# Performance work log

Hardware: AMD Instinct MI355X
Metric: run time of the kernel (lower is better)

Reference implementation:

```python
import jax, jax.numpy as jnp
import numpy as np

KS = 3
PAD = 1
STRIDE = 1


def conv2d(x, w, b, stride, pad):
    out = jax.lax.conv_general_dilated(
        x, w, (stride, stride), [(pad, pad), (pad, pad)],
        dimension_numbers=("NCHW", "OIHW", "NCHW"))
    if b is not None:
        out = out + b[None, :, None, None]
    return out


def setup_inputs() -> dict:
    key = jax.random.key(0)
    k = jax.random.split(key, 5)
    b, c, h, w = 4, 64, 128, 128
    return {
        "x0": jax.random.normal(k[0], (b, c, h, w), jnp.float32),
        "x1": jax.random.normal(k[1], (b, c, h, w), jnp.float32),
        "p_w": jax.random.normal(k[2], (2 * KS * KS, c, 3, 3), jnp.float32) * 0.01,
        "p_b": jax.random.normal(k[3], (2 * KS * KS,), jnp.float32) * 0.1,
        "conv_w": jax.random.normal(k[4], (64, c, KS, KS), jnp.float32) * 0.05,
    }


def _deform_forward(x0, x1, p_w, p_b, conv_w):
    ks, N = KS, KS * KS
    offset = conv2d(x1, p_w, p_b, STRIDE, 1)           # (b, 2N, h, w)
    b, _, h, w = offset.shape
    c = x0.shape[1]
    xp = jnp.pad(x0, ((0, 0), (0, 0), (PAD, PAD), (PAD, PAD)))
    Hp, Wp = xp.shape[2], xp.shape[3]

    # kernel-relative offsets p_n and base grid p_0 (1-indexed, as in torch code)
    r = jnp.arange(-(ks - 1) // 2, (ks - 1) // 2 + 1)
    pnx, pny = jnp.meshgrid(r, r, indexing="ij")
    p_n = jnp.concatenate([pnx.ravel(), pny.ravel()]).astype(offset.dtype).reshape(1, 2 * N, 1, 1)
    ax = jnp.arange(1, h * STRIDE + 1, STRIDE)
    ay = jnp.arange(1, w * STRIDE + 1, STRIDE)
    p0x, p0y = jnp.meshgrid(ax, ay, indexing="ij")    # (h, w)
    p_0 = jnp.concatenate([jnp.broadcast_to(p0x, (1, N, h, w)),
                           jnp.broadcast_to(p0y, (1, N, h, w))], 1).astype(offset.dtype)

    p = (p_0 + p_n + offset).transpose(0, 2, 3, 1)     # (b, h, w, 2N)
    q_lt = jnp.floor(jax.lax.stop_gradient(p))
    q_rb = q_lt + 1.0
    qltx = jnp.clip(q_lt[..., :N], 0, Hp - 1).astype(jnp.int32)
    qlty = jnp.clip(q_lt[..., N:], 0, Wp - 1).astype(jnp.int32)
    qrbx = jnp.clip(q_rb[..., :N], 0, Hp - 1).astype(jnp.int32)
    qrby = jnp.clip(q_rb[..., N:], 0, Wp - 1).astype(jnp.int32)
    px = jnp.clip(p[..., :N], 0, Hp - 1)
    py = jnp.clip(p[..., N:], 0, Wp - 1)

    fx_lt = qltx.astype(px.dtype); fy_lt = qlty.astype(px.dtype)
    fx_rb = qrbx.astype(px.dtype); fy_rb = qrby.astype(px.dtype)
    g_lt = (1 + (fx_lt - px)) * (1 + (fy_lt - py))
    g_rb = (1 - (fx_rb - px)) * (1 - (fy_rb - py))
    g_lb = (1 + (fx_lt - px)) * (1 - (fy_rb - py))
    g_rt = (1 - (fx_rb - px)) * (1 + (fy_lt - py))

    x_flat = xp.reshape(b, c, Hp * Wp)

    def gather(qx, qy):
        idx = qx * Wp + qy                              # (b, h, w, N)
        return jax.vmap(lambda xb, ib: xb[:, ib])(x_flat, idx)  # (b, c, h, w, N)

    x_lt = gather(qltx, qlty)
    x_rb = gather(qrbx, qrby)
    x_lb = gather(qltx, qrby)
    x_rt = gather(qrbx, qlty)

    x_off = (g_lt[:, None] * x_lt + g_rb[:, None] * x_rb +
             g_lb[:, None] * x_lb + g_rt[:, None] * x_rt)  # (b, c, h, w, N)

    # (b,c,h,w,ki,kj) -> (b,c,h*ks,w*ks)
    x_off = x_off.reshape(b, c, h, w, ks, ks).transpose(0, 1, 2, 4, 3, 5).reshape(b, c, h * ks, w * ks)
    return conv2d(x_off, conv_w, None, ks, 0)


def reference(x0, x1, p_w, p_b, conv_w):
    return _deform_forward(x0, x1, p_w, p_b, conv_w)
```

## Files before the change

### kernel.cpp

```cpp
#include <hip/hip_runtime.h>

#define BATCH 4
#define CH    64
#define HH    128
#define WW    128
#define HW    (HH*WW)
#define HP    130
#define NOFF  18
#define OC    64

typedef _Float16 half8 __attribute__((ext_vector_type(8)));
typedef _Float16 half2t __attribute__((ext_vector_type(2)));
typedef float f32x4 __attribute__((ext_vector_type(4)));

#define WF_OFF  0
#define PF_OFF  73728
#define X0T_OFF 110592
#define X1T_OFF 8763392
#define REC_OFF 17416192

__global__ __launch_bounds__(256) void prep_all(
    const float* __restrict__ x0, const float* __restrict__ x1,
    const float* __restrict__ cw, const float* __restrict__ pw,
    _Float16* __restrict__ x0t, _Float16* __restrict__ x1t,
    _Float16* __restrict__ wf, _Float16* __restrict__ pf) {
  int blk = blockIdx.x, tid = threadIdx.x;
  if (blk < 2048) {
    __shared__ float tile[64 * 66];
    int jh = blk & 1, i = (blk >> 1) & 127, b = (blk >> 8) & 3, which = blk >> 10;
    const float* src = which ? x1 : x0;
    _Float16* dst = which ? x1t : x0t;
#pragma unroll
    for (int it = 0; it < 4; it++) {
      int idx = it * 256 + tid;
      int c = idx >> 4, j4 = (idx & 15) << 2;
      float4 v = *(const float4*)(src + (size_t)(b * CH + c) * HW + i * WW + jh * 64 + j4);
      *(float4*)&tile[c * 66 + j4] = v;
    }
    __syncthreads();
    int jl = tid >> 2, cq = (tid & 3) << 4;
    _Float16* dp = dst + ((size_t)(b * HP + i + 1) * HP + (jh * 64 + jl + 1)) * CH + cq;
#pragma unroll
    for (int h = 0; h < 2; h++) {
      half8 v;
#pragma unroll
      for (int cc = 0; cc < 8; cc++) v[cc] = (_Float16)tile[(cq + h * 8 + cc) * 66 + jl];
      *(half8*)(dp + h * 8) = v;
    }
    if (tid < 8) {
      int jo = jh ? (HP - 1) : 0;
      _Float16* zp = dst + ((size_t)(b * HP + i + 1) * HP + jo) * CH + tid * 8;
      int4 z = {0, 0, 0, 0};
      *(int4*)zp = z;
    }
  } else if (blk < 2064) {
    int z = blk - 2048;
    int which = z >> 3, b = (z >> 1) & 3, top = z & 1;
    _Float16* dst = (which ? x1t : x0t) + ((size_t)(b * HP + top * (HP - 1)) * HP) * CH;
    int4 zz = {0, 0, 0, 0};
    for (int e = tid; e < 1040; e += 256) *(int4*)((char*)dst + e * 16) = zz;
  } else {
    int gid = (blk - 2064) * 256 + tid;
    if (gid < 36864) {
      int j = gid & 7, lane = (gid >> 3) & 63, mt = (gid >> 9) & 3, s = gid >> 11;
      int oc = mt * 16 + (lane & 15);
      int t = s * 32 + (lane >> 4) * 8 + j;
      int k = t >> 6, c = t & 63;
      wf[gid] = (_Float16)cw[(oc * CH + c) * 9 + k];
    } else {
      int g = gid - 36864;
      int j = g & 7, lane = (g >> 3) & 63, mt = (g >> 9) & 1, s = g >> 10;
      int o = mt * 16 + (lane & 15);
      int t = s * 32 + (lane >> 4) * 8 + j;
      int k = t >> 6, c = t & 63;
      pf[g] = (o < NOFF) ? (_Float16)pw[(o * CH + c) * 9 + k] : (_Float16)0.f;
    }
  }
}

__global__ __launch_bounds__(256, 4) void offset_recs(
    const _Float16* __restrict__ x1t, const _Float16* __restrict__ pf,
    const float* __restrict__ pb, int4* __restrict__ recs) {
  __shared__ _Float16 x1s[3 * 66 * 72];
  __shared__ float offs_lds[64 * 20];
  int blk = blockIdx.x;
  int jh2 = blk & 1, i = (blk >> 1) & 127, b = blk >> 8;
  int j0 = jh2 * 64;
  int tid = threadIdx.x, lane = tid & 63, nt = tid >> 6;
  const _Float16* x1b = x1t + (size_t)b * HP * HP * CH;

#pragma unroll
  for (int it = 0; it < 7; it++) {
    int tau = it * 256 + tid;
    if (tau < 1584) {
      int ki = tau / 528, r2 = tau - ki * 528;
      int col = r2 >> 3, cg = r2 & 7;
      half8 v = *(const half8*)(x1b + ((size_t)(i + ki) * HP + (j0 + col)) * CH + cg * 8);
      *(half8*)&x1s[(ki * 66 + col) * 72 + cg * 8] = v;
    }
  }
  __syncthreads();

  int p = lane & 15, q = lane >> 4;
  const half8* pfv = (const half8*)pf;
  f32x4 acc0 = {0.f, 0.f, 0.f, 0.f}, acc1 = {0.f, 0.f, 0.f, 0.f};
#pragma unroll 3
  for (int s = 0; s < 18; s++) {
    int u = 4 * s + q, k = u >> 3, c0 = (u & 7) << 3;
    int ki = (k * 86) >> 8, kj = k - ki * 3;
    half8 bfrag = *(const half8*)&x1s[(ki * 66 + nt * 16 + p + kj) * 72 + c0];
    acc0 = __builtin_amdgcn_mfma_f32_16x16x32_f16(pfv[(s * 2 + 0) * 64 + lane], bfrag, acc0, 0, 0, 0);
    acc1 = __builtin_amdgcn_mfma_f32_16x16x32_f16(pfv[(s * 2 + 1) * 64 + lane], bfrag, acc1, 0, 0, 0);
  }
  int col = lane & 15, quad = lane >> 4;
  int px = nt * 16 + col;
#pragma unroll
  for (int r = 0; r < 4; r++) {
    int o = quad * 4 + r;
    offs_lds[px * 20 + o] = acc0[r] + pb[o];
    int o2 = 16 + o;
    if (o2 < NOFF) offs_lds[px * 20 + o2] = acc1[r] + pb[o2];
  }
  __syncthreads();

  int px2 = tid >> 2, kg = tid & 3;
  int jj = j0 + px2;
#pragma unroll
  for (int t = 0; t < 3; t++) {
    int k = kg + t * 4;
    if (k <= 8) {
      float ox = offs_lds[px2 * 20 + k], oy = offs_lds[px2 * 20 + k + 9];
      int ki = (k * 86) >> 8, kj = k - ki * 3;
      float pxr = (float)(i + ki) + ox;
      float pyr = (float)(jj + kj) + oy;
      float fx = floorf(pxr), fy = floorf(pyr);
      float qltx = fminf(fmaxf(fx, 0.f), 129.f);
      float qlty = fminf(fmaxf(fy, 0.f), 129.f);
      float qrbx = fminf(fmaxf(fx + 1.f, 0.f), 129.f);
      float qrby = fminf(fmaxf(fy + 1.f, 0.f), 129.f);
      float pxc = fminf(fmaxf(pxr, 0.f), 129.f);
      float pyc = fminf(fmaxf(pyr, 0.f), 129.f);
      float glt = (1.f + qltx - pxc) * (1.f + qlty - pyc);
      float grb = (1.f - qrbx + pxc) * (1.f - qrby + pyc);
      float glb = (1.f + qltx - pxc) * (1.f - qrby + pyc);
      float grt = (1.f - qrbx + pxc) * (1.f + qlty - pyc);
      int4 rec;
      rec.x = (int)qltx | ((int)qlty << 16);
      rec.y = (int)qrbx | ((int)qrby << 16);
      half2t gA = {(_Float16)glt, (_Float16)grb};
      half2t gB = {(_Float16)glb, (_Float16)grt};
      rec.z = __builtin_bit_cast(int, gA);
      rec.w = __builtin_bit_cast(int, gB);
      recs[(size_t)((b * HH + i) * WW + jj) * 9 + k] = rec;
    }
  }
}

__global__ __launch_bounds__(256, 4) void deform_fused(
    const _Float16* __restrict__ x0t, const int4* __restrict__ recs,
    const _Float16* __restrict__ wf, float* __restrict__ out) {
  __shared__ __align__(16) _Float16 btile[2 * 18 * 64 * 8];

  int xcd = blockIdx.x & 7, local = blockIdx.x >> 3;
  int strip = xcd * 256 + local;
  int jq2 = strip & 3, i = (strip >> 2) & 127, b = strip >> 9;
  int j0 = jq2 * 32;
  int tid = threadIdx.x;
  const _Float16* x0b = x0t + (size_t)b * HP * HP * CH;

  {
    int cg = tid & 7, px = tid >> 3;
    int c0 = cg * 8;
    int nt = px >> 4, pxl = px & 15, kgq = cg & 3, sh = cg >> 2;
    const int4* recp = recs + (size_t)((b * HH + i) * WW + (j0 + px)) * 9;
    _Float16* wslot = &btile[(((nt * 18) * 4 + kgq) * 16 + pxl) * 8];
#pragma unroll
    for (int k = 0; k < 9; k++) {
      int4 rec = recp[k];
      int ltx = rec.x & 0xffff, lty = (int)((unsigned)rec.x >> 16);
      int rbx = rec.y & 0xffff, rby = (int)((unsigned)rec.y >> 16);
      const _Float16* rowl = x0b + (size_t)ltx * (HP * CH) + c0;
      const _Float16* rowr = x0b + (size_t)rbx * (HP * CH) + c0;
      half8 vlt = *(const half8*)(rowl + lty * CH);
      half8 vlb = *(const half8*)(rowl + rby * CH);
      half8 vrb = *(const half8*)(rowr + rby * CH);
      half8 vrt = *(const half8*)(rowr + lty * CH);
      half2t gA = __builtin_bit_cast(half2t, rec.z);
      half2t gB = __builtin_bit_cast(half2t, rec.w);
      half8 f = vlt * gA.x + vrb * gA.y + vlb * gB.x + vrt * gB.y;
      int s = k * 2 + sh;
      *(half8*)(wslot + s * 512) = f;
    }
  }
  __syncthreads();

  {
    int lane = tid & 63, w = tid >> 6;
    int nt = w & 1, mt0 = (w >> 1) * 2;
    f32x4 acc0 = {0.f, 0.f, 0.f, 0.f}, acc1 = {0.f, 0.f, 0.f, 0.f};
    const half8* wfv = (const half8*)wf;
    const half8* bt = (const half8*)&btile[nt * (18 * 512)];
#pragma unroll 6
    for (int s = 0; s < 18; s++) {
      half8 bfrag = bt[s * 64 + lane];
      acc0 = __builtin_amdgcn_mfma_f32_16x16x32_f16(wfv[(s * 4 + mt0) * 64 + lane], bfrag, acc0, 0, 0, 0);
      acc1 = __builtin_amdgcn_mfma_f32_16x16x32_f16(wfv[(s * 4 + mt0 + 1) * 64 + lane], bfrag, acc1, 0, 0, 0);
    }
    int col = lane & 15, quad = lane >> 4;
    int jo = j0 + nt * 16 + col;
#pragma unroll
    for (int r = 0; r < 4; r++) {
      int oc0 = mt0 * 16 + quad * 4 + r;
      int oc1 = (mt0 + 1) * 16 + quad * 4 + r;
      out[((b * OC + oc0) * HH + i) * WW + jo] = acc0[r];
      out[((b * OC + oc1) * HH + i) * WW + jo] = acc1[r];
    }
  }
}

extern "C" void kernel_launch(void* const* d_in, const int* in_sizes, int n_in,
                              void* d_out, int out_size, void* d_ws, size_t ws_size,
                              hipStream_t stream) {
  const float* x0 = (const float*)d_in[0];
  const float* x1 = (const float*)d_in[1];
  const float* pw = (const float*)d_in[2];
  const float* pb = (const float*)d_in[3];
  const float* cw = (const float*)d_in[4];
  float* out = (float*)d_out;

  _Float16* wfrag  = (_Float16*)((char*)d_ws + WF_OFF);
  _Float16* pwfrag = (_Float16*)((char*)d_ws + PF_OFF);
  _Float16* x0t    = (_Float16*)((char*)d_ws + X0T_OFF);
  _Float16* x1t    = (_Float16*)((char*)d_ws + X1T_OFF);
  int4*     recs   = (int4*)((char*)d_ws + REC_OFF);

  prep_all<<<dim3(2280), dim3(256), 0, stream>>>(x0, x1, cw, pw, x0t, x1t, wfrag, pwfrag);
  offset_recs<<<dim3(1024), dim3(256), 0, stream>>>(x1t, pwfrag, pb, recs);
  deform_fused<<<dim3(2048), dim3(256), 0, stream>>>(x0t, recs, wfrag, out);
}
```

Measured before the change: 120.9 us.

## Fuse offset convolution and bilinear record computation into deform kernel

Merges the offset-conv/record kernel into the deform kernel. Each block first computes the 18 offset channels for its 32-pixel strip with MFMA, reading x1 fragments straight from global memory instead of staging them in LDS. It then computes the bilinear indices and weights in registers before gathering. This removes one kernel launch and the write and read-back of the int4 records. The costs are redundant per-thread bilinear math (each of the 8 channel-group threads recomputes it), uncached global reads of x1 for the conv, and more work per block.

```diff
diff --git a/kernel.cpp b/kernel.cpp
--- a/kernel.cpp
+++ b/kernel.cpp
@@ -10,14 +10,12 @@
 #define OC    64
 
 typedef _Float16 half8 __attribute__((ext_vector_type(8)));
-typedef _Float16 half2t __attribute__((ext_vector_type(2)));
 typedef float f32x4 __attribute__((ext_vector_type(4)));
 
 #define WF_OFF  0
 #define PF_OFF  73728
 #define X0T_OFF 110592
 #define X1T_OFF 8763392
-#define REC_OFF 17416192
 
 __global__ __launch_bounds__(256) void prep_all(
     const float* __restrict__ x0, const float* __restrict__ x1,
@@ -78,61 +76,58 @@
   }
 }
 
-__global__ __launch_bounds__(256, 4) void offset_recs(
-    const _Float16* __restrict__ x1t, const _Float16* __restrict__ pf,
-    const float* __restrict__ pb, int4* __restrict__ recs) {
-  __shared__ _Float16 x1s[3 * 66 * 72];
-  __shared__ float offs_lds[64 * 20];
-  int blk = blockIdx.x;
-  int jh2 = blk & 1, i = (blk >> 1) & 127, b = blk >> 8;
-  int j0 = jh2 * 64;
-  int tid = threadIdx.x, lane = tid & 63, nt = tid >> 6;
+__global__ __launch_bounds__(256, 4) void deform_all(
+    const _Float16* __restrict__ x0t, const _Float16* __restrict__ x1t,
+    const _Float16* __restrict__ pf, const float* __restrict__ pb,
+    const _Float16* __restrict__ wf, float* __restrict__ out) {
+  __shared__ __align__(16) _Float16 btile[2 * 18 * 64 * 8];
+  __shared__ float offs[32 * 20];
+
+  int xcd = blockIdx.x & 7, local = blockIdx.x >> 3;
+  int strip = xcd * 256 + local;
+  int jq2 = strip & 3, i = (strip >> 2) & 127, b = strip >> 9;
+  int j0 = jq2 * 32;
+  int tid = threadIdx.x;
+  const _Float16* x0b = x0t + (size_t)b * HP * HP * CH;
   const _Float16* x1b = x1t + (size_t)b * HP * HP * CH;
 
+  {
+    int lane = tid & 63, w = tid >> 6;
+    int nt = w & 1, mt = w >> 1;
+    int p = lane & 15, q = lane >> 4;
+    int j = j0 + nt * 16 + p;
+    const half8* pfv = (const half8*)pf;
+    f32x4 acc = {0.f, 0.f, 0.f, 0.f};
+#pragma unroll 3
+    for (int s = 0; s < 18; s++) {
+      int u = 4 * s + q, k = u >> 3, c0 = (u & 7) << 3;
+      int ki = (k * 86) >> 8, kj = k - ki * 3;
+      half8 bfrag = *(const half8*)(x1b + ((size_t)(i + ki) * HP + (j + kj)) * CH + c0);
+      acc = __builtin_amdgcn_mfma_f32_16x16x32_f16(pfv[(s * 2 + mt) * 64 + lane], bfrag, acc, 0, 0, 0);
+    }
+    int col = lane & 15, quad = lane >> 4;
+    int px = nt * 16 + col;
 #pragma unroll
-  for (int it = 0; it < 7; it++) {
-    int tau = it * 256 + tid;
-    if (tau < 1584) {
-      int ki = tau / 528, r2 = tau - ki * 528;
-      int col = r2 >> 3, cg = r2 & 7;
-      half8 v = *(const half8*)(x1b + ((size_t)(i + ki) * HP + (j0 + col)) * CH + cg * 8);
-      *(half8*)&x1s[(ki * 66 + col) * 72 + cg * 8] = v;
+    for (int r = 0; r < 4; r++) {
+      int o = mt * 16 + quad * 4 + r;
+      if (o < NOFF) offs[px * 20 + o] = acc[r] + pb[o];
     }
   }
   __syncthreads();
 
-  int p = lane & 15, q = lane >> 4;
-  const half8* pfv = (const half8*)pf;
-  f32x4 acc0 = {0.f, 0.f, 0.f, 0.f}, acc1 = {0.f, 0.f, 0.f, 0.f};
-#pragma unroll 3
-  for (int s = 0; s < 18; s++) {
-    int u = 4 * s + q, k = u >> 3, c0 = (u & 7) << 3;
-    int ki = (k * 86) >> 8, kj = k - ki * 3;
-    half8 bfrag = *(const half8*)&x1s[(ki * 66 + nt * 16 + p + kj) * 72 + c0];
-    acc0 = __builtin_amdgcn_mfma_f32_16x16x32_f16(pfv[(s * 2 + 0) * 64 + lane], bfrag, acc0, 0, 0, 0);
-    acc1 = __builtin_amdgcn_mfma_f32_16x16x32_f16(pfv[(s * 2 + 1) * 64 + lane], bfrag, acc1, 0, 0, 0);
-  }
-  int col = lane & 15, quad = lane >> 4;
-  int px = nt * 16 + col;
+  {
+    int cg = tid & 7, px = tid >> 3;
+    int c0 = cg * 8;
+    int nt = px >> 4, pxl = px & 15, kgq = cg & 3, sh = cg >> 2;
+    int j = j0 + px;
+    _Float16* wslot = &btile[(((nt * 18) * 4 + kgq) * 16 + pxl) * 8];
 #pragma unroll
-  for (int r = 0; r < 4; r++) {
-    int o = quad * 4 + r;
-    offs_lds[px * 20 + o] = acc0[r] + pb[o];
-    int o2 = 16 + o;
-    if (o2 < NOFF) offs_lds[px * 20 + o2] = acc1[r] + pb[o2];
-  }
-  __syncthreads();
-
-  int px2 = tid >> 2, kg = tid & 3;
-  int jj = j0 + px2;
-#pragma unroll
-  for (int t = 0; t < 3; t++) {
-    int k = kg + t * 4;
-    if (k <= 8) {
-      float ox = offs_lds[px2 * 20 + k], oy = offs_lds[px2 * 20 + k + 9];
-      int ki = (k * 86) >> 8, kj = k - ki * 3;
+    for (int k = 0; k < 9; k++) {
+      float ox = offs[px * 20 + k];
+      float oy = offs[px * 20 + k + 9];
+      const int ki = k / 3, kj = k % 3;
       float pxr = (float)(i + ki) + ox;
-      float pyr = (float)(jj + kj) + oy;
+      float pyr = (float)(j + kj) + oy;
       float fx = floorf(pxr), fy = floorf(pyr);
       float qltx = fminf(fmaxf(fx, 0.f), 129.f);
       float qlty = fminf(fmaxf(fy, 0.f), 129.f);
@@ -144,50 +139,16 @@
       float grb = (1.f - qrbx + pxc) * (1.f - qrby + pyc);
       float glb = (1.f + qltx - pxc) * (1.f - qrby + pyc);
       float grt = (1.f - qrbx + pxc) * (1.f + qlty - pyc);
-      int4 rec;
-      rec.x = (int)qltx | ((int)qlty << 16);
-      rec.y = (int)qrbx | ((int)qrby << 16);
-      half2t gA = {(_Float16)glt, (_Float16)grb};
-      half2t gB = {(_Float16)glb, (_Float16)grt};
-      rec.z = __builtin_bit_cast(int, gA);
-      rec.w = __builtin_bit_cast(int, gB);
-      recs[(size_t)((b * HH + i) * WW + jj) * 9 + k] = rec;
-    }
-  }
-}
-
-__global__ __launch_bounds__(256, 4) void deform_fused(
-    const _Float16* __restrict__ x0t, const int4* __restrict__ recs,
-    const _Float16* __restrict__ wf, float* __restrict__ out) {
-  __shared__ __align__(16) _Float16 btile[2 * 18 * 64 * 8];
-
-  int xcd = blockIdx.x & 7, local = blockIdx.x >> 3;
-  int strip = xcd * 256 + local;
-  int jq2 = strip & 3, i = (strip >> 2) & 127, b = strip >> 9;
-  int j0 = jq2 * 32;
-  int tid = threadIdx.x;
-  const _Float16* x0b = x0t + (size_t)b * HP * HP * CH;
-
-  {
-    int cg = tid & 7, px = tid >> 3;
-    int c0 = cg * 8;
-    int nt = px >> 4, pxl = px & 15, kgq = cg & 3, sh = cg >> 2;
-    const int4* recp = recs + (size_t)((b * HH + i) * WW + (j0 + px)) * 9;
-    _Float16* wslot = &btile[(((nt * 18) * 4 + kgq) * 16 + pxl) * 8];
-#pragma unroll
-    for (int k = 0; k < 9; k++) {
-      int4 rec = recp[k];
-      int ltx = rec.x & 0xffff, lty = (int)((unsigned)rec.x >> 16);
-      int rbx = rec.y & 0xffff, rby = (int)((unsigned)rec.y >> 16);
+      int ltx = (int)qltx, lty = (int)qlty;
+      int rbx = (int)qrbx, rby = (int)qrby;
       const _Float16* rowl = x0b + (size_t)ltx * (HP * CH) + c0;
       const _Float16* rowr = x0b + (size_t)rbx * (HP * CH) + c0;
       half8 vlt = *(const half8*)(rowl + lty * CH);
       half8 vlb = *(const half8*)(rowl + rby * CH);
       half8 vrb = *(const half8*)(rowr + rby * CH);
       half8 vrt = *(const half8*)(rowr + lty * CH);
-      half2t gA = __builtin_bit_cast(half2t, rec.z);
-      half2t gB = __builtin_bit_cast(half2t, rec.w);
-      half8 f = vlt * gA.x + vrb * gA.y + vlb * gB.x + vrt * gB.y;
+      half8 f = vlt * (_Float16)glt + vrb * (_Float16)grb +
+                vlb * (_Float16)glb + vrt * (_Float16)grt;
       int s = k * 2 + sh;
       *(half8*)(wslot + s * 512) = f;
     }
@@ -232,9 +193,7 @@
   _Float16* pwfrag = (_Float16*)((char*)d_ws + PF_OFF);
   _Float16* x0t    = (_Float16*)((char*)d_ws + X0T_OFF);
   _Float16* x1t    = (_Float16*)((char*)d_ws + X1T_OFF);
-  int4*     recs   = (int4*)((char*)d_ws + REC_OFF);
 
   prep_all<<<dim3(2280), dim3(256), 0, stream>>>(x0, x1, cw, pw, x0t, x1t, wfrag, pwfrag);
-  offset_recs<<<dim3(1024), dim3(256), 0, stream>>>(x1t, pwfrag, pb, recs);
-  deform_fused<<<dim3(2048), dim3(256), 0, stream>>>(x0t, recs, wfrag, out);
+  deform_all<<<dim3(2048), dim3(256), 0, stream>>>(x0t, x1t, pwfrag, pb, wfrag, out);
 }
```

Result: slower. 126.8 us (+4.9%).
